# Optimization experiments

Hardware: AMD Instinct MI355X
Metric: run time of the kernel (lower is better)

## Reference

```python
import jax, jax.numpy as jnp
import numpy as np

N, F, G, E, L, HID, C = 16384, 256, 64, 131072, 3, 512, 2
EPS = 1e-5
IU = F * (F - 1) // 2      # 32640 strict-upper-tri features per graph
IN1 = IU + F * L           # 33408 MLP input width


def setup_inputs() -> dict:
    key = jax.random.key(0)
    ks = jax.random.split(key, 16)

    def w(k, shape, fan_in):
        return jax.random.normal(k, shape, jnp.float32) * (1.0 / np.sqrt(fan_in))

    return {
        "x": jax.random.normal(ks[0], (N, F), jnp.float32),
        "edge_index": jax.random.randint(ks[1], (2, E), 0, N, dtype=jnp.int32),
        "batch": jnp.repeat(jnp.arange(G, dtype=jnp.int32), N // G),  # F nodes per graph
        "lin_src_w": w(ks[2], (L, F, F), F), "lin_src_b": jnp.zeros((L, F), jnp.float32),
        "lin_dst_w": w(ks[3], (L, F, F), F), "lin_dst_b": jnp.zeros((L, F), jnp.float32),
        "att_w": w(ks[4], (L, 2 * F, 1), 2 * F), "att_b": jnp.zeros((L, 1), jnp.float32),
        "bn_g": jnp.ones((IU,), jnp.float32), "bn_b": jnp.zeros((IU,), jnp.float32),
        "bnh_g": jnp.ones((F * L,), jnp.float32), "bnh_b": jnp.zeros((F * L,), jnp.float32),
        "w1": w(ks[5], (IN1, HID), IN1), "b1": jnp.zeros((HID,), jnp.float32),
        "g1": jnp.ones((HID,), jnp.float32), "be1": jnp.zeros((HID,), jnp.float32),
        "w2": w(ks[6], (HID, HID // 2), HID), "b2": jnp.zeros((HID // 2,), jnp.float32),
        "g2": jnp.ones((HID // 2,), jnp.float32), "be2": jnp.zeros((HID // 2,), jnp.float32),
        "w3": w(ks[7], (HID // 2, HID // 2), HID // 2), "b3": jnp.zeros((HID // 2,), jnp.float32),
        "g3": jnp.ones((HID // 2,), jnp.float32), "be3": jnp.zeros((HID // 2,), jnp.float32),
        "w4": w(ks[8], (HID // 2, C), HID // 2), "b4": jnp.zeros((C,), jnp.float32),
    }


def _bn(z, g, b):
    # BatchNorm1d (training-mode batch stats, biased variance, as torch uses for normalization)
    m = jnp.mean(z, 0)
    v = jnp.var(z, 0)
    return (z - m) * jax.lax.rsqrt(v + EPS) * g + b


def _conv(x, src, dst, Ws, bs, Wd, bd, Wa, ba):
    # EdgeLevelAttention layer (heads=1): gather -> concat -> linear -> softmax(heads) -> weighted scatter-add
    x_src = x @ Ws + bs                      # [N, F]
    x_dst = x @ Wd + bd                      # [N, F]
    x_j = x_src[src]                         # [E2, F] source features per edge
    x_i = x_dst[dst]                         # [E2, F] destination features per edge
    alpha = jax.nn.softmax(jnp.concatenate([x_i, x_j], -1) @ Wa + ba, axis=1)  # [E2, 1] (all ones for heads=1)
    msg = x_i * alpha                        # message uses x_i, as in the source
    return jax.ops.segment_sum(msg, dst, num_segments=N)


def reference(x, edge_index, batch, lin_src_w, lin_src_b, lin_dst_w, lin_dst_b,
              att_w, att_b, bn_g, bn_b, bnh_g, bnh_b,
              w1, b1, g1, be1, w2, b2, g2, be2, w3, b3, g3, be3, w4, b4):
    loops = jnp.arange(N, dtype=edge_index.dtype)          # add_self_loops
    src = jnp.concatenate([edge_index[0], loops])
    dst = jnp.concatenate([edge_index[1], loops])

    h = x
    pooled = []
    cnt = jax.ops.segment_sum(jnp.ones((N, 1), x.dtype), batch, num_segments=G)
    for l in range(L):
        h = _conv(h, src, dst, lin_src_w[l], lin_src_b[l],
                  lin_dst_w[l], lin_dst_b[l], att_w[l], att_b[l])
        pooled.append(jax.ops.segment_sum(h, batch, num_segments=G) / cnt)  # global_mean_pool

    iu = np.triu_indices(F, k=1)
    xt = x.reshape(G, F, F)[:, iu[0], iu[1]]               # strict upper triangle per graph [G, IU]
    xt = _bn(xt, bn_g, bn_b)
    hh = _bn(jnp.concatenate(pooled, 1), bnh_g, bnh_b)     # [G, F*L]
    z = jnp.concatenate([xt, hh], 1)                       # [G, IN1]

    z = jax.nn.relu(_bn(z @ w1 + b1, g1, be1))
    z = jax.nn.relu(_bn(z @ w2 + b2, g2, be2))
    z = jax.nn.relu(_bn(z @ w3 + b3, g3, be3))
    return z @ w4 + b4                                     # [G, C]
```

## Files before the change

kernel.cpp:

```cpp
#include <hip/hip_runtime.h>
#include <cstdint>

typedef __attribute__((ext_vector_type(8))) short short8;
typedef __attribute__((ext_vector_type(4))) float f32x4;
typedef unsigned short ushort_t;

static constexpr int NN = 16384, FF = 256, GG = 64, EE = 131072, LL = 3;
static constexpr int HIDN = 512, IU = 32640, IN1 = 33408;
#define EPSV 1e-5f

__device__ inline unsigned short bf16r(float v) {
  unsigned u = __float_as_uint(v);
  u += 0x7FFFu + ((u >> 16) & 1u);
  return (unsigned short)(u >> 16);
}

__global__ __launch_bounds__(256) void k_zero(int* __restrict__ p) {
  int i = blockIdx.x * 256 + threadIdx.x;
  if (i < 16448) p[i] = 0;
}

__global__ __launch_bounds__(256) void k_hist(const int* __restrict__ dst,
                                              const int* __restrict__ batch,
                                              int* __restrict__ deg, int* __restrict__ cnt) {
  __shared__ int hist[64];
  int bx = blockIdx.x, t = threadIdx.x;
  if (bx < 512) {
    int e = bx * 256 + t;
    atomicAdd(&deg[dst[e]], 1);
  } else {
    if (t < 64) hist[t] = 0;
    __syncthreads();
    int4 v = ((const int4*)batch)[(bx - 512) * 256 + t];
    int a[4] = {v.x, v.y, v.z, v.w};
    int cur = a[0], run = 1;
#pragma unroll
    for (int j = 1; j < 4; ++j) {
      if (a[j] == cur) run++;
      else { atomicAdd(&hist[cur], run); cur = a[j]; run = 1; }
    }
    atomicAdd(&hist[cur], run);
    __syncthreads();
    if (t < 64 && hist[t]) atomicAdd(&cnt[t], hist[t]);
  }
}

template <int SIN>
__global__ __launch_bounds__(256, 2) void k_conv(const void* __restrict__ Ap,
                                                 const float* __restrict__ W,
                                                 const float* __restrict__ bias,
                                                 const int* __restrict__ deg,
                                                 unsigned* __restrict__ Cpk,
                                                 float* __restrict__ pooled_p, int lofs) {
  __shared__ __align__(16) unsigned short Ah[64][72], Al[64][72];
  __shared__ __align__(16) unsigned short Bh[128][72], Bl[128][72];
  int n0 = blockIdx.x * 128, m0 = blockIdx.y * 64;
  int t = threadIdx.x;
  int w = t >> 6, l = t & 63;
  int wn = w * 32;
  int lr = l & 15, lg = l >> 4;
  f32x4 acc[4][2];
#pragma unroll
  for (int fm = 0; fm < 4; ++fm)
#pragma unroll
    for (int fn = 0; fn < 2; ++fn) acc[fm][fn] = (f32x4){0.f, 0.f, 0.f, 0.f};

  int am = t >> 2, aq = t & 3;
  int bkp = t & 3, bnf = (t >> 2) & 31, brr = t >> 7;

  for (int ks = 0; ks < 4; ++ks) {
    int k0 = ks * 64;
    if (ks) __syncthreads();
    if (SIN == 0) {
      const float* ap = (const float*)Ap + (size_t)(m0 + am) * FF + k0;
#pragma unroll
      for (int i = 0; i < 4; ++i) {
        int k = aq * 4 + i * 16;
        float4 v = *(const float4*)(ap + k);
        const float* vf = (const float*)&v;
        unsigned short h[4], lo[4];
#pragma unroll
        for (int j = 0; j < 4; ++j) {
          h[j] = bf16r(vf[j]);
          lo[j] = bf16r(vf[j] - __uint_as_float((unsigned)h[j] << 16));
        }
        *(uint2*)&Ah[am][k] = make_uint2((unsigned)h[0] | ((unsigned)h[1] << 16),
                                         (unsigned)h[2] | ((unsigned)h[3] << 16));
        *(uint2*)&Al[am][k] = make_uint2((unsigned)lo[0] | ((unsigned)lo[1] << 16),
                                         (unsigned)lo[2] | ((unsigned)lo[3] << 16));
      }
    } else {
      const unsigned* ap = (const unsigned*)Ap + (size_t)(m0 + am) * FF + k0;
#pragma unroll
      for (int i = 0; i < 4; ++i) {
        int k = aq * 4 + i * 16;
        uint4 v = *(const uint4*)(ap + k);
        const unsigned* vu = (const unsigned*)&v;
        unsigned short h[4], lo[4];
#pragma unroll
        for (int j = 0; j < 4; ++j) {
          h[j] = (unsigned short)(vu[j] >> 16);
          lo[j] = (unsigned short)vu[j];
        }
        *(uint2*)&Ah[am][k] = make_uint2((unsigned)h[0] | ((unsigned)h[1] << 16),
                                         (unsigned)h[2] | ((unsigned)h[3] << 16));
        *(uint2*)&Al[am][k] = make_uint2((unsigned)lo[0] | ((unsigned)lo[1] << 16),
                                         (unsigned)lo[2] | ((unsigned)lo[3] << 16));
      }
    }
#pragma unroll
    for (int r2 = 0; r2 < 4; ++r2) {
      int k = 2 * bkp + 8 * (brr * 4 + r2);
      const float* wp = W + (size_t)(k0 + k) * FF + n0 + bnf * 4;
      float4 va = *(const float4*)wp;
      float4 vb = *(const float4*)(wp + FF);
      const float* fa = (const float*)&va;
      const float* fb = (const float*)&vb;
#pragma unroll
      for (int j = 0; j < 4; ++j) {
        unsigned short ha = bf16r(fa[j]), hb = bf16r(fb[j]);
        unsigned short la = bf16r(fa[j] - __uint_as_float((unsigned)ha << 16));
        unsigned short lb = bf16r(fb[j] - __uint_as_float((unsigned)hb << 16));
        int n = bnf * 4 + j;
        *(unsigned*)&Bh[n][k] = (unsigned)ha | ((unsigned)hb << 16);
        *(unsigned*)&Bl[n][k] = (unsigned)la | ((unsigned)lb << 16);
      }
    }
    __syncthreads();
#pragma unroll
    for (int k2 = 0; k2 < 2; ++k2) {
      int kk = k2 * 32 + lg * 8;
      short8 afh[4], afl[4], bfh[2], bfl[2];
#pragma unroll
      for (int fm = 0; fm < 4; ++fm) {
        afh[fm] = *(const short8*)&Ah[fm * 16 + lr][kk];
        afl[fm] = *(const short8*)&Al[fm * 16 + lr][kk];
      }
#pragma unroll
      for (int fn = 0; fn < 2; ++fn) {
        bfh[fn] = *(const short8*)&Bh[wn + fn * 16 + lr][kk];
        bfl[fn] = *(const short8*)&Bl[wn + fn * 16 + lr][kk];
      }
#pragma unroll
      for (int fm = 0; fm < 4; ++fm)
#pragma unroll
        for (int fn = 0; fn < 2; ++fn) {
          acc[fm][fn] = __builtin_amdgcn_mfma_f32_16x16x32_bf16(afl[fm], bfh[fn], acc[fm][fn], 0, 0, 0);
          acc[fm][fn] = __builtin_amdgcn_mfma_f32_16x16x32_bf16(afh[fm], bfl[fn], acc[fm][fn], 0, 0, 0);
          acc[fm][fn] = __builtin_amdgcn_mfma_f32_16x16x32_bf16(afh[fm], bfh[fn], acc[fm][fn], 0, 0, 0);
        }
    }
  }
  float degf[4][4];
#pragma unroll
  for (int fm = 0; fm < 4; ++fm)
#pragma unroll
    for (int r = 0; r < 4; ++r)
      degf[fm][r] = (float)(deg[m0 + fm * 16 + lg * 4 + r] + 1);
  int g = blockIdx.y >> 2, sub = blockIdx.y & 3;
#pragma unroll
  for (int fn = 0; fn < 2; ++fn) {
    int col = n0 + wn + fn * 16 + lr;
    float bb = bias[col];
    float cs = 0.f;
#pragma unroll
    for (int fm = 0; fm < 4; ++fm) {
      const float* av = (const float*)&acc[fm][fn];
#pragma unroll
      for (int r = 0; r < 4; ++r) {
        int row = m0 + fm * 16 + lg * 4 + r;
        float v = (av[r] + bb) * degf[fm][r];
        cs += v;
        if (Cpk) {
          unsigned uv = __float_as_uint(v);
          unsigned hi = uv & 0xFFFF0000u;
          unsigned short lo16 = bf16r(v - __uint_as_float(hi));
          Cpk[(size_t)row * FF + col] = hi | (unsigned)lo16;
        }
      }
    }
    cs += __shfl_xor(cs, 16);
    cs += __shfl_xor(cs, 32);
    if (lg == 0)
      pooled_p[((size_t)sub * 64 + g) * (FF * LL) + lofs + col] = cs;
  }
}

__global__ __launch_bounds__(1024, 1) void k_bn_front(const float* __restrict__ x,
                                                      const float* __restrict__ bn_g,
                                                      const float* __restrict__ bn_b,
                                                      const float* __restrict__ pooled_p,
                                                      const int* __restrict__ cnt,
                                                      const float* __restrict__ bnh_g,
                                                      const float* __restrict__ bnh_b,
                                                      ushort_t* __restrict__ zh,
                                                      ushort_t* __restrict__ zl) {
  if (blockIdx.x < 256) {
    __shared__ float sb1[16][256], sb2[16][256];
    __shared__ float rsA[256], bbA[256];
    int i = blockIdx.x, t = threadIdx.x;
    int jq = t & 63, gq = t >> 6;
    int j4 = jq * 4;
    float4 vals[4];
    float s1[4] = {}, s2[4] = {};
#pragma unroll
    for (int r = 0; r < 4; ++r) {
      int g = gq * 4 + r;
      float4 vv = *(const float4*)(x + (size_t)(g * 256 + i) * FF + j4);
      vals[r] = vv;
      s1[0] += vv.x; s2[0] += vv.x * vv.x;
      s1[1] += vv.y; s2[1] += vv.y * vv.y;
      s1[2] += vv.z; s2[2] += vv.z * vv.z;
      s1[3] += vv.w; s2[3] += vv.w * vv.w;
    }
    *(float4*)&sb1[gq][j4] = make_float4(s1[0], s1[1], s1[2], s1[3]);
    *(float4*)&sb2[gq][j4] = make_float4(s2[0], s2[1], s2[2], s2[3]);
    __syncthreads();
    if (t < 256) {
      int j = t;
      float S1 = 0.f, S2 = 0.f;
#pragma unroll
      for (int q = 0; q < 16; ++q) { S1 += sb1[q][j]; S2 += sb2[q][j]; }
      float m = S1 * (1.f / 64.f);
      float var = S2 * (1.f / 64.f) - m * m;
      float rs = 0.f, bb = 0.f;
      if (j > i) {
        int p = i * 255 - (i * (i - 1)) / 2 + (j - i - 1);
        rs = rsqrtf(var + EPSV) * bn_g[p];
        bb = bn_b[p] - m * rs;
      }
      rsA[j] = rs;
      bbA[j] = bb;
    }
    __syncthreads();
    int P0 = i * 255 - (i * (i - 1)) / 2 - i - 1;
#pragma unroll
    for (int r = 0; r < 4; ++r) {
      int g = gq * 4 + r;
      size_t base = (size_t)g * IN1 + P0;
      const float* vf = (const float*)&vals[r];
#pragma unroll
      for (int jj = 0; jj < 4; ++jj) {
        int j = j4 + jj;
        if (j > i) {
          float f = vf[jj] * rsA[j] + bbA[j];
          unsigned short h = bf16r(f);
          zh[base + j] = h;
          zl[base + j] = bf16r(f - __uint_as_float((unsigned)h << 16));
        }
      }
    }
  } else {
    __shared__ float pb1[4][64], pb2[4][64], prs[64], pbb[64];
    int t = threadIdx.x;
    if (t >= 256) return;
    int bx = blockIdx.x - 256;
    int ql = t & 63, gq = t >> 6;
    int q = bx * 64 + ql;
    float vals[16];
    float s1 = 0.f, s2 = 0.f;
#pragma unroll
    for (int gg = 0; gg < 16; ++gg) {
      int g = gq * 16 + gg;
      float v = (pooled_p[((size_t)0 * 64 + g) * (FF * LL) + q] +
                 pooled_p[((size_t)1 * 64 + g) * (FF * LL) + q] +
                 pooled_p[((size_t)2 * 64 + g) * (FF * LL) + q] +
                 pooled_p[((size_t)3 * 64 + g) * (FF * LL) + q]) / (float)cnt[g];
      vals[gg] = v;
      s1 += v;
      s2 += v * v;
    }
    pb1[gq][ql] = s1;
    pb2[gq][ql] = s2;
    __syncthreads();
    if (t < 64) {
      float S1 = pb1[0][t] + pb1[1][t] + pb1[2][t] + pb1[3][t];
      float S2 = pb2[0][t] + pb2[1][t] + pb2[2][t] + pb2[3][t];
      float m = S1 * (1.f / 64.f);
      float var = S2 * (1.f / 64.f) - m * m;
      int qq = bx * 64 + t;
      float rs = rsqrtf(var + EPSV) * bnh_g[qq];
      prs[t] = rs;
      pbb[t] = bnh_b[qq] - m * rs;
    }
    __syncthreads();
#pragma unroll
    for (int gg = 0; gg < 16; ++gg) {
      int g = gq * 16 + gg;
      float f = vals[gg] * prs[ql] + pbb[ql];
      unsigned short h = bf16r(f);
      zh[(size_t)g * IN1 + IU + q] = h;
      zl[(size_t)g * IN1 + IU + q] = bf16r(f - __uint_as_float((unsigned)h << 16));
    }
  }
}

__global__ __launch_bounds__(256, 4) void k_w1(const ushort_t* __restrict__ zh,
                                               const ushort_t* __restrict__ zl,
                                               const float* __restrict__ W,
                                               float* __restrict__ partial) {
  __shared__ __align__(16) unsigned short Zh[64][72], Zl[64][72];
  __shared__ __align__(16) unsigned short Wh[64][72], Wl[64][72];
  int nb = blockIdx.x, s = blockIdx.y;
  int t = threadIdx.x;
  int w = t >> 6, l = t & 63, lr = l & 15, lg = l >> 4;
  int ncol = nb * 64 + w * 16 + lr;
  f32x4 acc[4];
#pragma unroll
  for (int mt = 0; mt < 4; ++mt) acc[mt] = (f32x4){0.f, 0.f, 0.f, 0.f};

  for (int c = s; c < 522; c += 64) {
    int p0 = c * 64;
    if (c != s) __syncthreads();
#pragma unroll
    for (int it = 0; it < 2; ++it) {
      int idx = it * 256 + t;
      int g = idx >> 3, kq = idx & 7;
      *(uint4*)&Zh[g][kq * 8] = *(const uint4*)(zh + (size_t)g * IN1 + p0 + kq * 8);
      *(uint4*)&Zl[g][kq * 8] = *(const uint4*)(zl + (size_t)g * IN1 + p0 + kq * 8);
    }
#pragma unroll
    for (int it = 0; it < 2; ++it) {
      int idx = it * 256 + t;
      int kp = idx >> 4, cg = idx & 15;
      int k = kp * 2;
      const float* wp = W + (size_t)(p0 + k) * HIDN + nb * 64 + cg * 4;
      float4 va = *(const float4*)wp;
      float4 vb = *(const float4*)(wp + HIDN);
      const float* fa = (const float*)&va;
      const float* fb = (const float*)&vb;
#pragma unroll
      for (int j = 0; j < 4; ++j) {
        unsigned ua = __float_as_uint(fa[j]);
        unsigned ub = __float_as_uint(fb[j]);
        unsigned short ha = (unsigned short)(ua >> 16);
        unsigned short hb = (unsigned short)(ub >> 16);
        unsigned short la = bf16r(fa[j] - __uint_as_float(ua & 0xFFFF0000u));
        unsigned short lb = bf16r(fb[j] - __uint_as_float(ub & 0xFFFF0000u));
        int col = cg * 4 + j;
        *(unsigned*)&Wh[col][k] = (unsigned)ha | ((unsigned)hb << 16);
        *(unsigned*)&Wl[col][k] = (unsigned)la | ((unsigned)lb << 16);
      }
    }
    __syncthreads();
#pragma unroll
    for (int k2 = 0; k2 < 2; ++k2) {
      int kloc = k2 * 32 + lg * 8;
      short8 bh = *(const short8*)&Wh[w * 16 + lr][kloc];
      short8 bl = *(const short8*)&Wl[w * 16 + lr][kloc];
#pragma unroll
      for (int mt = 0; mt < 4; ++mt) {
        short8 ah = *(const short8*)&Zh[mt * 16 + lr][kloc];
        short8 al = *(const short8*)&Zl[mt * 16 + lr][kloc];
        acc[mt] = __builtin_amdgcn_mfma_f32_16x16x32_bf16(al, bh, acc[mt], 0, 0, 0);
        acc[mt] = __builtin_amdgcn_mfma_f32_16x16x32_bf16(ah, bl, acc[mt], 0, 0, 0);
        acc[mt] = __builtin_amdgcn_mfma_f32_16x16x32_bf16(ah, bh, acc[mt], 0, 0, 0);
      }
    }
  }
#pragma unroll
  for (int mt = 0; mt < 4; ++mt) {
    const float* av = (const float*)&acc[mt];
#pragma unroll
    for (int r = 0; r < 4; ++r) {
      int g = mt * 16 + lg * 4 + r;
      partial[((size_t)s * 64 + g) * HIDN + ncol] = av[r];
    }
  }
}

__global__ __launch_bounds__(256) void k_reduce(const float* __restrict__ partial,
                                                const float* __restrict__ bias,
                                                float* __restrict__ out, int S, int N) {
  int idx = blockIdx.x * 256 + threadIdx.x;
  if (idx >= 64 * N) return;
  int h = idx % N;
  float a = bias[h];
  for (int s = 0; s < S; ++s) a += partial[(size_t)s * 64 * N + idx];
  out[idx] = a;
}

template <int INBN>
__global__ __launch_bounds__(256, 2) void k_mlp_small(const float* __restrict__ Z,
                                                      const float* __restrict__ ibn_g,
                                                      const float* __restrict__ ibn_b,
                                                      const float* __restrict__ W,
                                                      const float* __restrict__ bias,
                                                      const float* __restrict__ gamma,
                                                      const float* __restrict__ beta,
                                                      float* __restrict__ out, int K, int N) {
  __shared__ float Ws[512 * 16];
  __shared__ float zl[64][132];
  __shared__ float sb1[16][17], sb2[16][17];
  int t = threadIdx.x;
  int h0 = blockIdx.x * 16;
  for (int idx = t; idx < K * 4; idx += 256) {
    int r = idx >> 2, q = idx & 3;
    *(float4*)&Ws[r * 16 + q * 4] = *(const float4*)(W + (size_t)r * N + h0 + q * 4);
  }
  int c = t & 15, gq = t >> 4;
  float acc[4] = {};
  for (int ch = 0; ch < K; ch += 128) {
    for (int idx = t; idx < 64 * 32; idx += 256) {
      int g = idx >> 5, kq = idx & 31;
      *(float4*)&zl[g][kq * 4] = *(const float4*)(Z + (size_t)g * K + ch + kq * 4);
    }
    __syncthreads();
    if (INBN) {
      if (t < 128) {
        float s1 = 0.f, s2 = 0.f;
#pragma unroll
        for (int g = 0; g < 64; ++g) {
          float v = zl[g][t];
          s1 += v;
          s2 += v * v;
        }
        float m = s1 * (1.f / 64.f);
        float var = s2 * (1.f / 64.f) - m * m;
        float rs = rsqrtf(var + EPSV) * ibn_g[ch + t];
        float bb = ibn_b[ch + t] - m * rs;
#pragma unroll
        for (int g = 0; g < 64; ++g)
          zl[g][t] = fmaxf(zl[g][t] * rs + bb, 0.f);
      }
      __syncthreads();
    }
#pragma unroll 8
    for (int kk = 0; kk < 128; ++kk) {
      float w = Ws[(ch + kk) * 16 + c];
#pragma unroll
      for (int i = 0; i < 4; ++i) acc[i] = fmaf(zl[gq * 4 + i][kk], w, acc[i]);
    }
    __syncthreads();
  }
  float bb = bias[h0 + c];
  float s1 = 0.f, s2 = 0.f;
#pragma unroll
  for (int i = 0; i < 4; ++i) {
    acc[i] += bb;
    s1 += acc[i];
    s2 += acc[i] * acc[i];
  }
  sb1[gq][c] = s1;
  sb2[gq][c] = s2;
  __syncthreads();
  float S1 = 0.f, S2 = 0.f;
#pragma unroll
  for (int q = 0; q < 16; ++q) { S1 += sb1[q][c]; S2 += sb2[q][c]; }
  float m = S1 * (1.f / 64.f);
  float var = S2 * (1.f / 64.f) - m * m;
  float rs = rsqrtf(var + EPSV) * gamma[h0 + c];
  float be = beta[h0 + c];
#pragma unroll
  for (int i = 0; i < 4; ++i)
    out[(size_t)(gq * 4 + i) * N + h0 + c] = fmaxf((acc[i] - m) * rs + be, 0.f);
}

__global__ __launch_bounds__(256) void k_final(const float* __restrict__ A,
                                               const float* __restrict__ w4,
                                               const float* __restrict__ b4,
                                               float* __restrict__ out) {
  __shared__ float w4l[512];
  int t = threadIdx.x;
  w4l[t] = w4[t];
  w4l[256 + t] = w4[256 + t];
  __syncthreads();
  int w = t >> 6, l = t & 63;
  for (int g = w * 16; g < w * 16 + 16; ++g) {
    float4 av = *(const float4*)(A + (size_t)g * 256 + l * 4);
    float c0 = av.x * w4l[(l * 4 + 0) * 2] + av.y * w4l[(l * 4 + 1) * 2] +
               av.z * w4l[(l * 4 + 2) * 2] + av.w * w4l[(l * 4 + 3) * 2];
    float c1 = av.x * w4l[(l * 4 + 0) * 2 + 1] + av.y * w4l[(l * 4 + 1) * 2 + 1] +
               av.z * w4l[(l * 4 + 2) * 2 + 1] + av.w * w4l[(l * 4 + 3) * 2 + 1];
#pragma unroll
    for (int o = 32; o > 0; o >>= 1) {
      c0 += __shfl_xor(c0, o);
      c1 += __shfl_xor(c1, o);
    }
    if (l == 0) {
      out[g * 2 + 0] = c0 + b4[0];
      out[g * 2 + 1] = c1 + b4[1];
    }
  }
}

extern "C" void kernel_launch(void* const* d_in, const int* in_sizes, int n_in,
                              void* d_out, int out_size, void* d_ws, size_t ws_size,
                              hipStream_t stream) {
  const float* x = (const float*)d_in[0];
  const int* edge = (const int*)d_in[1];
  const int* batch = (const int*)d_in[2];
  const float* lin_dst_w = (const float*)d_in[5];
  const float* lin_dst_b = (const float*)d_in[6];
  const float* bn_g = (const float*)d_in[9];
  const float* bn_b = (const float*)d_in[10];
  const float* bnh_g = (const float*)d_in[11];
  const float* bnh_b = (const float*)d_in[12];
  const float* w1 = (const float*)d_in[13];
  const float* b1 = (const float*)d_in[14];
  const float* g1 = (const float*)d_in[15];
  const float* be1 = (const float*)d_in[16];
  const float* w2 = (const float*)d_in[17];
  const float* b2 = (const float*)d_in[18];
  const float* g2 = (const float*)d_in[19];
  const float* be2 = (const float*)d_in[20];
  const float* w3 = (const float*)d_in[21];
  const float* b3 = (const float*)d_in[22];
  const float* g3 = (const float*)d_in[23];
  const float* be3 = (const float*)d_in[24];
  const float* w4 = (const float*)d_in[25];
  const float* b4 = (const float*)d_in[26];
  const int* dstp = edge + EE;

  char* ws = (char*)d_ws;
  int* deg = (int*)(ws);
  int* cnt = (int*)(ws + 65536);
  float* bufA = (float*)(ws + 131072);
  float* bufB = (float*)(ws + 131072 + 16777216);
  float* pooled_p = (float*)(ws + 131072 + 2 * 16777216);
  char* tail = ws + 131072 + 2 * 16777216 + 786432;
  float* m1 = (float*)(tail);
  float* m2b = (float*)(tail + 131072);
  float* m3b = (float*)(tail + 131072 + 65536);
  ushort_t* zh = (ushort_t*)bufA;
  ushort_t* zlp = zh + (size_t)64 * IN1;
  float* partial = bufB;

  k_zero<<<65, 256, 0, stream>>>(deg);
  k_hist<<<528, 256, 0, stream>>>(dstp, batch, deg, cnt);

  k_conv<0><<<dim3(2, 256), 256, 0, stream>>>(x, lin_dst_w, lin_dst_b, deg,
                                              (unsigned*)bufA, pooled_p, 0);
  k_conv<1><<<dim3(2, 256), 256, 0, stream>>>(bufA, lin_dst_w + (size_t)FF * FF,
                                              lin_dst_b + FF, deg, (unsigned*)bufB,
                                              pooled_p, FF);
  k_conv<1><<<dim3(2, 256), 256, 0, stream>>>(bufB, lin_dst_w + (size_t)2 * FF * FF,
                                              lin_dst_b + 2 * FF, deg, (unsigned*)nullptr,
                                              pooled_p, 2 * FF);

  k_bn_front<<<268, 1024, 0, stream>>>(x, bn_g, bn_b, pooled_p, cnt, bnh_g, bnh_b, zh, zlp);

  k_w1<<<dim3(8, 64), 256, 0, stream>>>(zh, zlp, w1, partial);
  k_reduce<<<128, 256, 0, stream>>>(partial, b1, m1, 64, HIDN);

  k_mlp_small<1><<<16, 256, 0, stream>>>(m1, g1, be1, w2, b2, g2, be2, m2b, HIDN, 256);
  k_mlp_small<0><<<16, 256, 0, stream>>>(m2b, nullptr, nullptr, w3, b3, g3, be3, m3b, 256, 256);

  k_final<<<1, 256, 0, stream>>>(m3b, w4, b4, (float*)d_out);
}
```

Baseline: 173.2 us.

## Pre-split conv weights to bf16 hi/lo once and shrink conv N-tile to 64

A prologue kernel (merged with the degree-zeroing launch) splits all three layers' lin_dst weights into bf16 high/low halves once and stores them in workspace. The conv GEMM kernels then load these pre-split halves instead of converting fp32 weights in every block. The output tile is narrowed from 128 to 64 columns, which doubles the grid, halves LDS and accumulators per block, and raises the occupancy hint to 4. The cost is an extra launch pass over the weights and more reloading of A tiles across the larger grid.

```diff
diff --git a/kernel.cpp b/kernel.cpp
--- a/kernel.cpp
+++ b/kernel.cpp
@@ -15,9 +15,21 @@
   return (unsigned short)(u >> 16);
 }
 
-__global__ __launch_bounds__(256) void k_zero(int* __restrict__ p) {
-  int i = blockIdx.x * 256 + threadIdx.x;
-  if (i < 16448) p[i] = 0;
+__global__ __launch_bounds__(256) void k_pre(int* __restrict__ p,
+                                             const float* __restrict__ lw,
+                                             ushort_t* __restrict__ wh,
+                                             ushort_t* __restrict__ wl) {
+  int bx = blockIdx.x, t = threadIdx.x;
+  if (bx < 65) {
+    int i = bx * 256 + t;
+    if (i < 16448) p[i] = 0;
+  } else {
+    int idx = (bx - 65) * 256 + t;
+    float v = lw[idx];
+    unsigned short h = bf16r(v);
+    wh[idx] = h;
+    wl[idx] = bf16r(v - __uint_as_float((unsigned)h << 16));
+  }
 }
 
 __global__ __launch_bounds__(256) void k_hist(const int* __restrict__ dst,
@@ -46,27 +58,26 @@
 }
 
 template <int SIN>
-__global__ __launch_bounds__(256, 2) void k_conv(const void* __restrict__ Ap,
-                                                 const float* __restrict__ W,
+__global__ __launch_bounds__(256, 4) void k_conv(const void* __restrict__ Ap,
+                                                 const ushort_t* __restrict__ Wh3,
+                                                 const ushort_t* __restrict__ Wl3,
                                                  const float* __restrict__ bias,
                                                  const int* __restrict__ deg,
                                                  unsigned* __restrict__ Cpk,
                                                  float* __restrict__ pooled_p, int lofs) {
   __shared__ __align__(16) unsigned short Ah[64][72], Al[64][72];
-  __shared__ __align__(16) unsigned short Bh[128][72], Bl[128][72];
-  int n0 = blockIdx.x * 128, m0 = blockIdx.y * 64;
+  __shared__ __align__(16) unsigned short Bh[64][72], Bl[64][72];
+  int n0 = blockIdx.x * 64, m0 = blockIdx.y * 64;
   int t = threadIdx.x;
   int w = t >> 6, l = t & 63;
-  int wn = w * 32;
+  int wn = w * 16;
   int lr = l & 15, lg = l >> 4;
-  f32x4 acc[4][2];
-#pragma unroll
-  for (int fm = 0; fm < 4; ++fm)
-#pragma unroll
-    for (int fn = 0; fn < 2; ++fn) acc[fm][fn] = (f32x4){0.f, 0.f, 0.f, 0.f};
+  f32x4 acc[4];
+#pragma unroll
+  for (int fm = 0; fm < 4; ++fm) acc[fm] = (f32x4){0.f, 0.f, 0.f, 0.f};
 
   int am = t >> 2, aq = t & 3;
-  int bkp = t & 3, bnf = (t >> 2) & 31, brr = t >> 7;
+  int bkp = t & 3, bnf = (t >> 2) & 15, brr = t >> 6;
 
   for (int ks = 0; ks < 4; ++ks) {
     int k0 = ks * 64;
@@ -109,46 +120,39 @@
       }
     }
 #pragma unroll
-    for (int r2 = 0; r2 < 4; ++r2) {
-      int k = 2 * bkp + 8 * (brr * 4 + r2);
-      const float* wp = W + (size_t)(k0 + k) * FF + n0 + bnf * 4;
-      float4 va = *(const float4*)wp;
-      float4 vb = *(const float4*)(wp + FF);
-      const float* fa = (const float*)&va;
-      const float* fb = (const float*)&vb;
+    for (int r2 = 0; r2 < 2; ++r2) {
+      int k = 2 * bkp + 8 * (brr * 2 + r2);
+      const ushort_t* whp = Wh3 + (size_t)(k0 + k) * FF + n0 + bnf * 4;
+      const ushort_t* wlp = Wl3 + (size_t)(k0 + k) * FF + n0 + bnf * 4;
+      uint2 wha = *(const uint2*)whp;
+      uint2 whb = *(const uint2*)(whp + FF);
+      uint2 wla = *(const uint2*)wlp;
+      uint2 wlb = *(const uint2*)(wlp + FF);
+      const ushort_t* pha = (const ushort_t*)&wha;
+      const ushort_t* phb = (const ushort_t*)&whb;
+      const ushort_t* pla = (const ushort_t*)&wla;
+      const ushort_t* plb = (const ushort_t*)&wlb;
 #pragma unroll
       for (int j = 0; j < 4; ++j) {
-        unsigned short ha = bf16r(fa[j]), hb = bf16r(fb[j]);
-        unsigned short la = bf16r(fa[j] - __uint_as_float((unsigned)ha << 16));
-        unsigned short lb = bf16r(fb[j] - __uint_as_float((unsigned)hb << 16));
         int n = bnf * 4 + j;
-        *(unsigned*)&Bh[n][k] = (unsigned)ha | ((unsigned)hb << 16);
-        *(unsigned*)&Bl[n][k] = (unsigned)la | ((unsigned)lb << 16);
+        *(unsigned*)&Bh[n][k] = (unsigned)pha[j] | ((unsigned)phb[j] << 16);
+        *(unsigned*)&Bl[n][k] = (unsigned)pla[j] | ((unsigned)plb[j] << 16);
       }
     }
     __syncthreads();
 #pragma unroll
     for (int k2 = 0; k2 < 2; ++k2) {
       int kk = k2 * 32 + lg * 8;
-      short8 afh[4], afl[4], bfh[2], bfl[2];
+      short8 bh = *(const short8*)&Bh[wn + lr][kk];
+      short8 bl = *(const short8*)&Bl[wn + lr][kk];
 #pragma unroll
       for (int fm = 0; fm < 4; ++fm) {
-        afh[fm] = *(const short8*)&Ah[fm * 16 + lr][kk];
-        afl[fm] = *(const short8*)&Al[fm * 16 + lr][kk];
-      }
-#pragma unroll
-      for (int fn = 0; fn < 2; ++fn) {
-        bfh[fn] = *(const short8*)&Bh[wn + fn * 16 + lr][kk];
-        bfl[fn] = *(const short8*)&Bl[wn + fn * 16 + lr][kk];
-      }
-#pragma unroll
-      for (int fm = 0; fm < 4; ++fm)
-#pragma unroll
-        for (int fn = 0; fn < 2; ++fn) {
-          acc[fm][fn] = __builtin_amdgcn_mfma_f32_16x16x32_bf16(afl[fm], bfh[fn], acc[fm][fn], 0, 0, 0);
-          acc[fm][fn] = __builtin_amdgcn_mfma_f32_16x16x32_bf16(afh[fm], bfl[fn], acc[fm][fn], 0, 0, 0);
-          acc[fm][fn] = __builtin_amdgcn_mfma_f32_16x16x32_bf16(afh[fm], bfh[fn], acc[fm][fn], 0, 0, 0);
-        }
+        short8 ah = *(const short8*)&Ah[fm * 16 + lr][kk];
+        short8 al = *(const short8*)&Al[fm * 16 + lr][kk];
+        acc[fm] = __builtin_amdgcn_mfma_f32_16x16x32_bf16(al, bh, acc[fm], 0, 0, 0);
+        acc[fm] = __builtin_amdgcn_mfma_f32_16x16x32_bf16(ah, bl, acc[fm], 0, 0, 0);
+        acc[fm] = __builtin_amdgcn_mfma_f32_16x16x32_bf16(ah, bh, acc[fm], 0, 0, 0);
+      }
     }
   }
   float degf[4][4];
@@ -158,32 +162,29 @@
     for (int r = 0; r < 4; ++r)
       degf[fm][r] = (float)(deg[m0 + fm * 16 + lg * 4 + r] + 1);
   int g = blockIdx.y >> 2, sub = blockIdx.y & 3;
-#pragma unroll
-  for (int fn = 0; fn < 2; ++fn) {
-    int col = n0 + wn + fn * 16 + lr;
-    float bb = bias[col];
-    float cs = 0.f;
-#pragma unroll
-    for (int fm = 0; fm < 4; ++fm) {
-      const float* av = (const float*)&acc[fm][fn];
-#pragma unroll
-      for (int r = 0; r < 4; ++r) {
-        int row = m0 + fm * 16 + lg * 4 + r;
-        float v = (av[r] + bb) * degf[fm][r];
-        cs += v;
-        if (Cpk) {
-          unsigned uv = __float_as_uint(v);
-          unsigned hi = uv & 0xFFFF0000u;
-          unsigned short lo16 = bf16r(v - __uint_as_float(hi));
-          Cpk[(size_t)row * FF + col] = hi | (unsigned)lo16;
-        }
-      }
-    }
-    cs += __shfl_xor(cs, 16);
-    cs += __shfl_xor(cs, 32);
-    if (lg == 0)
-      pooled_p[((size_t)sub * 64 + g) * (FF * LL) + lofs + col] = cs;
-  }
+  int col = n0 + wn + lr;
+  float bb = bias[col];
+  float cs = 0.f;
+#pragma unroll
+  for (int fm = 0; fm < 4; ++fm) {
+    const float* av = (const float*)&acc[fm];
+#pragma unroll
+    for (int r = 0; r < 4; ++r) {
+      int row = m0 + fm * 16 + lg * 4 + r;
+      float v = (av[r] + bb) * degf[fm][r];
+      cs += v;
+      if (Cpk) {
+        unsigned uv = __float_as_uint(v);
+        unsigned hi = uv & 0xFFFF0000u;
+        unsigned short lo16 = bf16r(v - __uint_as_float(hi));
+        Cpk[(size_t)row * FF + col] = hi | (unsigned)lo16;
+      }
+    }
+  }
+  cs += __shfl_xor(cs, 16);
+  cs += __shfl_xor(cs, 32);
+  if (lg == 0)
+    pooled_p[((size_t)sub * 64 + g) * (FF * LL) + lofs + col] = cs;
 }
 
 __global__ __launch_bounds__(1024, 1) void k_bn_front(const float* __restrict__ x,
@@ -518,7 +519,9 @@
   float* bufA = (float*)(ws + 131072);
   float* bufB = (float*)(ws + 131072 + 16777216);
   float* pooled_p = (float*)(ws + 131072 + 2 * 16777216);
-  char* tail = ws + 131072 + 2 * 16777216 + 786432;
+  ushort_t* wh3 = (ushort_t*)(ws + 131072 + 2 * 16777216 + 786432);
+  ushort_t* wl3 = wh3 + (size_t)LL * FF * FF;
+  char* tail = ws + 131072 + 2 * 16777216 + 786432 + 786432;
   float* m1 = (float*)(tail);
   float* m2b = (float*)(tail + 131072);
   float* m3b = (float*)(tail + 131072 + 65536);
@@ -526,17 +529,17 @@
   ushort_t* zlp = zh + (size_t)64 * IN1;
   float* partial = bufB;
 
-  k_zero<<<65, 256, 0, stream>>>(deg);
+  k_pre<<<833, 256, 0, stream>>>(deg, lin_dst_w, wh3, wl3);
   k_hist<<<528, 256, 0, stream>>>(dstp, batch, deg, cnt);
 
-  k_conv<0><<<dim3(2, 256), 256, 0, stream>>>(x, lin_dst_w, lin_dst_b, deg,
+  k_conv<0><<<dim3(4, 256), 256, 0, stream>>>(x, wh3, wl3, lin_dst_b, deg,
                                               (unsigned*)bufA, pooled_p, 0);
-  k_conv<1><<<dim3(2, 256), 256, 0, stream>>>(bufA, lin_dst_w + (size_t)FF * FF,
-                                              lin_dst_b + FF, deg, (unsigned*)bufB,
-                                              pooled_p, FF);
-  k_conv<1><<<dim3(2, 256), 256, 0, stream>>>(bufB, lin_dst_w + (size_t)2 * FF * FF,
-                                              lin_dst_b + 2 * FF, deg, (unsigned*)nullptr,
-                                              pooled_p, 2 * FF);
+  k_conv<1><<<dim3(4, 256), 256, 0, stream>>>(bufA, wh3 + (size_t)FF * FF,
+                                              wl3 + (size_t)FF * FF, lin_dst_b + FF, deg,
+                                              (unsigned*)bufB, pooled_p, FF);
+  k_conv<1><<<dim3(4, 256), 256, 0, stream>>>(bufB, wh3 + (size_t)2 * FF * FF,
+                                              wl3 + (size_t)2 * FF * FF, lin_dst_b + 2 * FF,
+                                              deg, (unsigned*)nullptr, pooled_p, 2 * FF);
 
   k_bn_front<<<268, 1024, 0, stream>>>(x, bn_g, bn_b, pooled_p, cnt, bnh_g, bnh_b, zh, zlp);
 
```

Measured after the change: 187.1 us. +8.0%, slower.
